# Kernel optimization log

Measured on AMD Instinct MI355X. Metric: run time of the kernel, lower is better.

The kernel has to match this reference:

```python
import jax, jax.numpy as jnp
import numpy as np
import math

B, S, D, H = 2, 2048, 1024, 16
DH = D // H

def setup_inputs() -> dict:
    key = jax.random.key(0)
    k = jax.random.split(key, 6)
    scale = 1.0 / math.sqrt(D)
    x = jax.random.normal(k[0], (B, S, D), jnp.float32)
    mask = jnp.ones((B, S), jnp.int32)
    # torch.nn.Linear weights: [out_features, in_features]
    W_q = jax.random.normal(k[1], (D, D), jnp.float32) * scale
    b_q = jnp.zeros((D,), jnp.float32)
    W_v = jax.random.normal(k[2], (D, D), jnp.float32) * scale
    W_out = jax.random.normal(k[3], (D, D), jnp.float32) * scale
    b_out = jnp.zeros((D,), jnp.float32)
    return {"x": x, "W_q": W_q, "b_q": b_q, "W_v": W_v, "W_out": W_out, "b_out": b_out, "mask": mask}

def reference(x, W_q, b_q, W_v, W_out, b_out, mask):
    inv_sqrt_dh = 1.0 / math.sqrt(DH)
    # q: [B, H, S, DH]
    q = (x @ W_q.T + b_q).reshape(B, S, H, DH).transpose(0, 2, 1, 3)
    # L2-distance attention logits: -(||q_s||^2 - 2 q_s.q_t + ||q_t||^2)/sqrt(dh)
    sq = jnp.sum(q * q, axis=-1)  # [B, H, S]
    qk = jnp.einsum('bhsd,bhtd->bhst', q, q)  # [B, H, S, S]
    logits = -(sq[..., :, None] - 2.0 * qk + sq[..., None, :]) * inv_sqrt_dh
    logits = jnp.where(mask[:, None, None, :] == 0, jnp.float32(-9e15), logits)
    w = jax.nn.softmax(logits, axis=-1)  # [B, H, S, S]
    # W_q_T[h, j, i] = W_q[i, h*DH + j] -> [H, DH, D]
    W_q_T = W_q.reshape(D, H, DH).transpose(1, 2, 0)
    # v[h, i, j] = W_v[i, h*DH + j] -> [H, D, DH]
    v = W_v.reshape(D, H, DH).transpose(1, 0, 2)
    attn = jnp.einsum('bhst,bhtd->bhsd', w, q)          # [B, H, S, DH]
    attn = jnp.einsum('bhsd,hde->bhse', attn, W_q_T)    # [B, H, S, D]
    attn = jnp.einsum('bhse,hef->bhsf', attn, v) * inv_sqrt_dh  # [B, H, S, DH]
    attn = attn.transpose(0, 2, 1, 3).reshape(B, S, D)
    return x + attn @ W_out.T + b_out
```

## Files before the change

### kernel.cpp

```cpp
#include <hip/hip_runtime.h>

#define S_LEN 2048
#define D_DIM 1024
#define NH    16
#define DHEAD 64

typedef float f32x4 __attribute__((ext_vector_type(4)));
typedef __bf16 bf16x8 __attribute__((ext_vector_type(8)));
typedef unsigned short u16;
typedef unsigned int u32;
typedef unsigned short u16x8 __attribute__((ext_vector_type(8)));
typedef unsigned short u16x4 __attribute__((ext_vector_type(4)));

__device__ __forceinline__ u16 f2bf(float f) {
    union { float f; unsigned u; } c; c.f = f;
    unsigned u = c.u + 0x7fffu + ((c.u >> 16) & 1u);
    return (u16)(u >> 16);
}

__device__ __forceinline__ u32 cvtpk(float lo, float hi) {
    u32 r;
    asm("v_cvt_pk_bf16_f32 %0, %1, %2" : "=v"(r) : "v"(lo), "v"(hi));
    return r;
}

__device__ __forceinline__ u32 pack_bf(float lo, float hi) {
    union { float f; u32 u; } a, b; a.f = lo; b.f = hi;
    return (b.u & 0xFFFF0000u) | (a.u >> 16);
}

#if __has_builtin(__builtin_amdgcn_exp2f)
#define EXP2(x) __builtin_amdgcn_exp2f(x)
#else
#define EXP2(x) exp2f(x)
#endif

#define C_QK  0.36067376022224085f
#define C_SQ  0.18033688011112043f

#define MFMA16(a, b, c) __builtin_amdgcn_mfma_f32_16x16x32_bf16((a), (b), (c), 0, 0, 0)

__global__ __launch_bounds__(256) void k_prep(
    const float* __restrict__ x, const float* __restrict__ Wq,
    u16* __restrict__ xbf, u16* __restrict__ Wqbf) {
    const size_t NX = (size_t)2 * S_LEN * D_DIM / 8;
    const size_t NW = (size_t)D_DIM * D_DIM / 8;
    for (size_t c = (size_t)blockIdx.x * 256 + threadIdx.x; c < NX + NW;
         c += (size_t)gridDim.x * 256) {
        const float* src; u16* dst; size_t off;
        if (c < NX) { src = x;  dst = xbf;  off = c * 8; }
        else        { src = Wq; dst = Wqbf; off = (c - NX) * 8; }
        f32x4 a = *(const f32x4*)(src + off);
        f32x4 b = *(const f32x4*)(src + off + 4);
        union { u32 w[4]; u16x8 v; } o;
        o.w[0] = cvtpk(a[0], a[1]); o.w[1] = cvtpk(a[2], a[3]);
        o.w[2] = cvtpk(b[0], b[1]); o.w[3] = cvtpk(b[2], b[3]);
        *(u16x8*)(dst + off) = o.v;
    }
}

__global__ __launch_bounds__(512, 4) void k_mega1(
    const u16* __restrict__ xbf, const u16* __restrict__ Wqbf,
    const float* __restrict__ Wq, const float* __restrict__ Wv,
    const float* __restrict__ bq, const int* __restrict__ mask,
    u16* __restrict__ Qbf, u16* __restrict__ QT,
    float* __restrict__ sq05, float* __restrict__ Mpart) {
    __shared__ __align__(16) char smem[38912];
    const int tid = threadIdx.x;

    if (blockIdx.x >= 256) {
        const int id = blockIdx.x - 256;
        const int z = id & 7, h = id >> 3;
        float* Qp = (float*)smem;
        float* Vp = (float*)(smem + 16384);
        const int r = tid >> 3, seg = tid & 7;
        const int j0 = (tid >> 4) * 2;
        const int f0 = (tid & 15) * 4;
        f32x4 acc0 = {0.f, 0.f, 0.f, 0.f}, acc1 = acc0;
        for (int c = 0; c < 2; ++c) {
            const int e0 = z * 128 + c * 64;
            __syncthreads();
            const float* q = Wq + (size_t)(e0 + r) * D_DIM + h * DHEAD + seg * 8;
            const float* v = Wv + (size_t)(e0 + r) * D_DIM + h * DHEAD + seg * 8;
            *(f32x4*)&Qp[r * 64 + seg * 8]     = *(const f32x4*)q;
            *(f32x4*)&Qp[r * 64 + seg * 8 + 4] = *(const f32x4*)(q + 4);
            *(f32x4*)&Vp[r * 64 + seg * 8]     = *(const f32x4*)v;
            *(f32x4*)&Vp[r * 64 + seg * 8 + 4] = *(const f32x4*)(v + 4);
            __syncthreads();
#pragma unroll 8
            for (int e = 0; e < 64; ++e) {
                float q0 = Qp[e * 64 + j0], q1 = Qp[e * 64 + j0 + 1];
                f32x4 vv = *(const f32x4*)&Vp[e * 64 + f0];
                acc0 += q0 * vv;
                acc1 += q1 * vv;
            }
        }
        float* dst = Mpart + (size_t)z * 65536 + ((size_t)(h * 64 + j0)) * 64 + f0;
        *(f32x4*)dst        = acc0 * 0.125f;
        *(f32x4*)(dst + 64) = acc1 * 0.125f;
        return;
    }

    u16* Al = (u16*)smem;
    u16* Bl = (u16*)(smem + 18432);
    float* sqp = (float*)(smem + 36864);

    const int lane = tid & 63, w = tid >> 6;
    const int wm = w & 1, wn = w >> 1;
    const int col16 = lane & 15, quad = lane >> 4;
    const int bm = blockIdx.x & 31, bn = blockIdx.x >> 5;

    f32x4 acc[4][2];
    const f32x4 z4 = {0.f, 0.f, 0.f, 0.f};
#pragma unroll
    for (int i = 0; i < 4; ++i)
#pragma unroll
        for (int j = 0; j < 2; ++j) acc[i][j] = z4;

    const int ar = tid >> 2, as = tid & 3;
    const u16* pa = xbf + (size_t)(bm * 128 + ar) * D_DIM + as * 16;
    const u16* pb = Wqbf + (size_t)(bn * 128 + ar) * D_DIM + as * 16;

    u16x8 ra[2], rb[2];
#pragma unroll
    for (int i = 0; i < 2; ++i) ra[i] = *(const u16x8*)(pa + i * 8);
#pragma unroll
    for (int i = 0; i < 2; ++i) rb[i] = *(const u16x8*)(pb + i * 8);

    for (int k0 = 0; k0 < D_DIM; k0 += 64) {
        __syncthreads();
#pragma unroll
        for (int i = 0; i < 2; ++i) *(u16x8*)&Al[ar * 72 + as * 16 + i * 8] = ra[i];
#pragma unroll
        for (int i = 0; i < 2; ++i) *(u16x8*)&Bl[ar * 72 + as * 16 + i * 8] = rb[i];
        __syncthreads();
        if (k0 + 64 < D_DIM) {
#pragma unroll
            for (int i = 0; i < 2; ++i) ra[i] = *(const u16x8*)(pa + k0 + 64 + i * 8);
#pragma unroll
            for (int i = 0; i < 2; ++i) rb[i] = *(const u16x8*)(pb + k0 + 64 + i * 8);
        }
#pragma unroll
        for (int kh = 0; kh < 2; ++kh) {
            bf16x8 af[4];
#pragma unroll
            for (int mt = 0; mt < 4; ++mt)
                af[mt] = *(const bf16x8*)&Al[(wm * 64 + mt * 16 + col16) * 72 + kh * 32 + quad * 8];
#pragma unroll
            for (int nt = 0; nt < 2; ++nt) {
                bf16x8 bfr = *(const bf16x8*)&Bl[(wn * 32 + nt * 16 + col16) * 72 + kh * 32 + quad * 8];
#pragma unroll
                for (int mt = 0; mt < 4; ++mt)
                    acc[mt][nt] = MFMA16(af[mt], bfr, acc[mt][nt]);
            }
        }
    }

    const int hh = wn >> 1;
    f32x4 ssum[4];
#pragma unroll
    for (int mt = 0; mt < 4; ++mt) ssum[mt] = z4;

    u16 qv16[2][4][4];
#pragma unroll
    for (int nt = 0; nt < 2; ++nt) {
        int col = bn * 128 + wn * 32 + nt * 16 + col16;
        float bqv = bq[col];
#pragma unroll
        for (int mt = 0; mt < 4; ++mt) {
            int row0 = bm * 128 + wm * 64 + mt * 16 + quad * 4;
#pragma unroll
            for (int rr = 0; rr < 4; ++rr) {
                float qv = acc[mt][nt][rr] + bqv;
                ssum[mt][rr] += qv * qv;
                u16 bv = f2bf(qv);
                qv16[nt][mt][rr] = bv;
                Qbf[(size_t)(row0 + rr) * D_DIM + col] = bv;
            }
        }
    }
    float vred[4][4];
#pragma unroll
    for (int mt = 0; mt < 4; ++mt)
#pragma unroll
        for (int rr = 0; rr < 4; ++rr) {
            float v = ssum[mt][rr];
            v += __shfl_xor(v, 1); v += __shfl_xor(v, 2);
            v += __shfl_xor(v, 4); v += __shfl_xor(v, 8);
            vred[mt][rr] = v;
        }
    if (col16 == 0) {
#pragma unroll
        for (int mt = 0; mt < 4; ++mt)
#pragma unroll
            for (int rr = 0; rr < 4; ++rr)
                sqp[wn * 128 + wm * 64 + mt * 16 + quad * 4 + rr] = vred[mt][rr];
    }
    __syncthreads();

    u16* Td = (u16*)smem;
#pragma unroll
    for (int nt = 0; nt < 2; ++nt) {
        int dloc = (wn & 1) * 32 + nt * 16 + col16;
#pragma unroll
        for (int mt = 0; mt < 4; ++mt) {
            int sl = wm * 64 + mt * 16 + quad * 4;
#pragma unroll
            for (int rr = 0; rr < 4; ++rr)
                Td[(hh * 64 + dloc) * 130 + sl + rr] = qv16[nt][mt][rr];
        }
    }
    __syncthreads();

    const int bb = (bm * 128) >> 11, s0 = (bm * 128) & 2047;
    if (tid < 256) {
        int r = tid & 127, hh2 = tid >> 7;
        float v = sqp[(2 * hh2) * 128 + r] + sqp[(2 * hh2 + 1) * 128 + r];
        int sidx = s0 + r;
        float o = mask[bb * S_LEN + sidx] ? v * C_SQ : 1e30f;
        sq05[((size_t)(bb * NH + bn * 2 + hh2)) * S_LEN + sidx] = o;
    }
    {
        int dr = tid >> 2, ch = tid & 3;
        int hh3 = dr >> 6, d = dr & 63;
        u16* dst = QT + ((size_t)(bb * NH + bn * 2 + hh3) * DHEAD + d) * S_LEN + s0 + ch * 32;
        const u16* src = Td + (hh3 * 64 + d) * 130 + ch * 32;
#pragma unroll
        for (int i = 0; i < 4; ++i)
            *(u16x8*)(dst + i * 8) = *(const u16x8*)(src + i * 8);
    }
}

__global__ __launch_bounds__(256, 2) void k_mega2(
    const u16* __restrict__ Qbf, const u16* __restrict__ QT,
    const float* __restrict__ sq05, u16* __restrict__ attnO,
    const float* __restrict__ Mpart, const float* __restrict__ Wout,
    u16* __restrict__ W2) {
    __shared__ __align__(16) char smem[34816];
    const int tid = threadIdx.x;

    if (blockIdx.x >= 512) {
        const int id = blockIdx.x - 512;
        const int ob = id & 15, h = id >> 4;
        float* Ms = (float*)smem;
        float* Ws = (float*)(smem + 16640);
        {
            int rr = tid >> 2, seg = tid & 3;
            const size_t mo = ((size_t)(h * 64 + rr)) * 64 + seg * 16;
            const float* ws = Wout + (size_t)(ob * 64 + rr) * D_DIM + h * DHEAD + seg * 16;
#pragma unroll
            for (int e = 0; e < 16; ++e) {
                float s = 0.f;
#pragma unroll
                for (int k = 0; k < 8; ++k) s += Mpart[mo + e + (size_t)k * 65536];
                Ms[rr * 65 + seg * 16 + e] = s;
                Ws[rr * 65 + seg * 16 + e] = ws[e];
            }
        }
        __syncthreads();
        int j = tid & 63, o0 = (tid >> 6) * 16;
        for (int oo = o0; oo < o0 + 16; ++oo) {
            float acc = 0.f;
#pragma unroll
            for (int f = 0; f < 64; ++f) acc += Ms[j * 65 + f] * Ws[oo * 65 + f];
            W2[(size_t)(ob * 64 + oo) * D_DIM + h * DHEAD + j] = f2bf(acc);
        }
        return;
    }

    u16* Kt  = (u16*)smem;
    u16* KtT = (u16*)(smem + 16384);
    float* sql = (float*)(smem + 32768);

    const int lane = tid & 63, w = tid >> 6;
    const int col16 = lane & 15, quad = lane >> 4;
    const int wq = w & 1, wk = w >> 1;
    const int bh = blockIdx.x & 31;
    const int qt = blockIdx.x >> 5;
    const int h = bh & 15;
    const int b = bh >> 4;
    const u16* qbase = Qbf + (size_t)b * S_LEN * D_DIM + h * DHEAD;
    const u16* qtbase = QT + ((size_t)(b * NH + h)) * DHEAD * S_LEN;
    const float* sqb = sq05 + ((size_t)(b * NH + h)) * S_LEN;

    bf16x8 qb[4][2];
#pragma unroll
    for (int nq = 0; nq < 4; ++nq)
#pragma unroll
        for (int k0 = 0; k0 < 2; ++k0)
            qb[nq][k0] = *(const bf16x8*)(qbase +
                (size_t)(qt * 128 + wq * 64 + nq * 16 + col16) * D_DIM + k0 * 32 + quad * 8);

    const int r00 = wk * 64 + (col16 >> 2) * 8 + (col16 & 3);
    const int swzA = (col16 & 3) | (((col16 >> 2) & 1) << 2);
    const int krow00 = r00 * 64 + (quad ^ swzA) * 8;
    const int sq00 = wk * 64 + quad * 8;
    int vrow[4];
#pragma unroll
    for (int dblk = 0; dblk < 4; ++dblk) {
        int rT = dblk * 16 + col16;
        vrow[dblk] = rT * 128 + ((wk * 8 + quad) ^ (rT & 7)) * 8;
    }

    const int kr = tid >> 1, ks = tid & 1;
    const int td = tid >> 2, ts = tid & 3;
    const int kswz = (kr & 3) | (((kr >> 3) & 1) << 2);
    const int tswz = td & 7;
    const u16* ksrc = qbase + (size_t)kr * D_DIM + ks * 32;
    const u16* tsrc = qtbase + (size_t)td * S_LEN + ts * 32;

    u16x8 pk[4], pt[4];
    float sv = 0.f;
#pragma unroll
    for (int i = 0; i < 4; ++i) pk[i] = *(const u16x8*)(ksrc + i * 8);
#pragma unroll
    for (int i = 0; i < 4; ++i) pt[i] = *(const u16x8*)(tsrc + i * 8);
    if (tid < 128) sv = sqb[tid];

    f32x4 Oacc[4][4], lacc[4];
    const f32x4 z4 = {0.f, 0.f, 0.f, 0.f};
#pragma unroll
    for (int n = 0; n < 4; ++n) {
        lacc[n] = z4;
#pragma unroll
        for (int d = 0; d < 4; ++d) Oacc[d][n] = z4;
    }
    bf16x8 ones;
    {
        union { u16x8 u; bf16x8 b; } cv;
#pragma unroll
        for (int e = 0; e < 8; ++e) cv.u[e] = 0x3F80;
        ones = cv.b;
    }

    for (int j = 0; j < S_LEN / 128; ++j) {
        __syncthreads();
#pragma unroll
        for (int i = 0; i < 4; ++i)
            *(u16x8*)(Kt + kr * 64 + ((ks * 4 + i) ^ kswz) * 8) = pk[i];
#pragma unroll
        for (int i = 0; i < 4; ++i)
            *(u16x8*)(KtT + td * 128 + ((ts * 4 + i) ^ tswz) * 8) = pt[i];
        if (tid < 128) sql[tid] = sv;
        __syncthreads();

        int jn = (j + 1) & 15;
        {
            const u16* kn = ksrc + (size_t)jn * 128 * D_DIM;
            const u16* tn = tsrc + (size_t)jn * 128;
#pragma unroll
            for (int i = 0; i < 4; ++i) pk[i] = *(const u16x8*)(kn + i * 8);
#pragma unroll
            for (int i = 0; i < 4; ++i) pt[i] = *(const u16x8*)(tn + i * 8);
            if (tid < 128) sv = sqb[jn * 128 + tid];
        }

        for (int kt = 0; kt < 2; ++kt) {
            f32x4 sacc[2][4];
#pragma unroll
            for (int kbh = 0; kbh < 2; ++kbh)
#pragma unroll
                for (int nq = 0; nq < 4; ++nq) sacc[kbh][nq] = z4;
#pragma unroll
            for (int kbh = 0; kbh < 2; ++kbh) {
                int kro = krow00 + kt * 2048 + kbh * 256;
                bf16x8 a0 = *(const bf16x8*)(Kt + kro);
                bf16x8 a1 = *(const bf16x8*)(Kt + (kro ^ 32));
#pragma unroll
                for (int nq = 0; nq < 4; ++nq) {
                    sacc[kbh][nq] = MFMA16(a0, qb[nq][0], sacc[kbh][nq]);
                    sacc[kbh][nq] = MFMA16(a1, qb[nq][1], sacc[kbh][nq]);
                }
            }

            bf16x8 va[4];
#pragma unroll
            for (int dblk = 0; dblk < 4; ++dblk)
                va[dblk] = *(const bf16x8*)(KtT + (vrow[dblk] ^ (kt * 32)));

            u32 pf[4][4];
#pragma unroll
            for (int kbh = 0; kbh < 2; ++kbh) {
                f32x4 sqv = *(const f32x4*)(sql + sq00 + kt * 32 + kbh * 4);
#pragma unroll
                for (int nq = 0; nq < 4; ++nq) {
                    float p0 = EXP2(fmaf(sacc[kbh][nq][0], C_QK, -sqv[0]));
                    float p1 = EXP2(fmaf(sacc[kbh][nq][1], C_QK, -sqv[1]));
                    float p2 = EXP2(fmaf(sacc[kbh][nq][2], C_QK, -sqv[2]));
                    float p3 = EXP2(fmaf(sacc[kbh][nq][3], C_QK, -sqv[3]));
                    pf[nq][kbh * 2]     = pack_bf(p0, p1);
                    pf[nq][kbh * 2 + 1] = pack_bf(p2, p3);
                }
            }

#pragma unroll
            for (int nq = 0; nq < 4; ++nq) {
                union { u32 u[4]; bf16x8 b; } pb;
#pragma unroll
                for (int i = 0; i < 4; ++i) pb.u[i] = pf[nq][i];
                lacc[nq] = MFMA16(ones, pb.b, lacc[nq]);
#pragma unroll
                for (int dblk = 0; dblk < 4; ++dblk)
                    Oacc[dblk][nq] = MFMA16(va[dblk], pb.b, Oacc[dblk][nq]);
            }
        }
    }

    __syncthreads();
    float* Obuf = (float*)smem;
    float* lred = (float*)(smem + 32768);
    if (wk == 1) {
#pragma unroll
        for (int dblk = 0; dblk < 4; ++dblk)
#pragma unroll
            for (int nq = 0; nq < 4; ++nq)
                *(f32x4*)(Obuf + ((wq * 16 + dblk * 4 + nq) * 64 + lane) * 4) = Oacc[dblk][nq];
#pragma unroll
        for (int nq = 0; nq < 4; ++nq)
            lred[(wq * 4 + nq) * 64 + lane] = lacc[nq][0];
    }
    __syncthreads();
    if (wk == 0) {
        float rinv[4];
#pragma unroll
        for (int nq = 0; nq < 4; ++nq)
            rinv[nq] = 1.f / (lacc[nq][0] + lred[(wq * 4 + nq) * 64 + lane]);
        u16* obase = attnO + (size_t)b * S_LEN * D_DIM + h * DHEAD;
#pragma unroll
        for (int dblk = 0; dblk < 4; ++dblk)
#pragma unroll
            for (int nq = 0; nq < 4; ++nq) {
                f32x4 o = Oacc[dblk][nq] + *(const f32x4*)(Obuf + ((wq * 16 + dblk * 4 + nq) * 64 + lane) * 4);
                int q = qt * 128 + wq * 64 + nq * 16 + col16;
                u16x4 pkk;
#pragma unroll
                for (int rr = 0; rr < 4; ++rr) pkk[rr] = f2bf(o[rr] * rinv[nq]);
                *(u16x4*)(obase + (size_t)q * D_DIM + dblk * 16 + quad * 4) = pkk;
            }
    }
}

__global__ __launch_bounds__(256, 4) void k_oproj(
    const u16* __restrict__ attnO, const u16* __restrict__ W2,
    const float* __restrict__ x, const float* __restrict__ bout, float* __restrict__ out) {
    __shared__ __align__(16) char smem[27648];
    u16* Al = (u16*)smem;
    u16* Bl = (u16*)(smem + 9216);
    const int tid = threadIdx.x, lane = tid & 63, wn = tid >> 6;
    const int col16 = lane & 15, quad = lane >> 4;
    const int bm = blockIdx.x, bn = blockIdx.y;

    f32x4 acc[4][2];
    const f32x4 z4 = {0.f, 0.f, 0.f, 0.f};
#pragma unroll
    for (int i = 0; i < 4; ++i)
#pragma unroll
        for (int j = 0; j < 2; ++j) acc[i][j] = z4;

    const int arA = tid >> 2, asA = tid & 3;
    const int brB = tid >> 1, bsB = tid & 1;
    const u16* pa = attnO + (size_t)(bm * 64 + arA) * D_DIM + asA * 16;
    const u16* pb = W2 + (size_t)(bn * 128 + brB) * D_DIM + bsB * 32;

    u16x8 ra[2], rb[4];
#pragma unroll
    for (int i = 0; i < 2; ++i) ra[i] = *(const u16x8*)(pa + i * 8);
#pragma unroll
    for (int i = 0; i < 4; ++i) rb[i] = *(const u16x8*)(pb + i * 8);

    for (int k0 = 0; k0 < D_DIM; k0 += 64) {
        __syncthreads();
#pragma unroll
        for (int i = 0; i < 2; ++i) *(u16x8*)&Al[arA * 72 + asA * 16 + i * 8] = ra[i];
#pragma unroll
        for (int i = 0; i < 4; ++i) *(u16x8*)&Bl[brB * 72 + bsB * 32 + i * 8] = rb[i];
        __syncthreads();
        if (k0 + 64 < D_DIM) {
#pragma unroll
            for (int i = 0; i < 2; ++i) ra[i] = *(const u16x8*)(pa + k0 + 64 + i * 8);
#pragma unroll
            for (int i = 0; i < 4; ++i) rb[i] = *(const u16x8*)(pb + k0 + 64 + i * 8);
        }
#pragma unroll
        for (int kh = 0; kh < 2; ++kh) {
            bf16x8 af[4];
#pragma unroll
            for (int mt = 0; mt < 4; ++mt)
                af[mt] = *(const bf16x8*)&Al[(mt * 16 + col16) * 72 + kh * 32 + quad * 8];
#pragma unroll
            for (int nt = 0; nt < 2; ++nt) {
                bf16x8 bfr = *(const bf16x8*)&Bl[(wn * 32 + nt * 16 + col16) * 72 + kh * 32 + quad * 8];
#pragma unroll
                for (int mt = 0; mt < 4; ++mt)
                    acc[mt][nt] = MFMA16(af[mt], bfr, acc[mt][nt]);
            }
        }
    }
#pragma unroll
    for (int nt = 0; nt < 2; ++nt) {
        int col = bn * 128 + wn * 32 + nt * 16 + col16;
        float bv = bout[col];
#pragma unroll
        for (int mt = 0; mt < 4; ++mt) {
            int row0 = bm * 64 + mt * 16 + quad * 4;
#pragma unroll
            for (int rr = 0; rr < 4; ++rr) {
                size_t idx = (size_t)(row0 + rr) * D_DIM + col;
                out[idx] = acc[mt][nt][rr] + x[idx] + bv;
            }
        }
    }
}

extern "C" void kernel_launch(void* const* d_in, const int* in_sizes, int n_in,
                              void* d_out, int out_size, void* d_ws, size_t ws_size,
                              hipStream_t stream) {
    const float* x    = (const float*)d_in[0];
    const float* Wq   = (const float*)d_in[1];
    const float* bq   = (const float*)d_in[2];
    const float* Wv   = (const float*)d_in[3];
    const float* Wout = (const float*)d_in[4];
    const float* bout = (const float*)d_in[5];
    const int*   mask = (const int*)d_in[6];
    float* out = (float*)d_out;

    char* ws = (char*)d_ws;
    u16*   Qbf   = (u16*)(ws);
    u16*   QT    = (u16*)(ws + (8u << 20));
    u16*   attnO = (u16*)(ws + (16u << 20));
    u16*   W2    = (u16*)(ws + (24u << 20));
    float* Mpart = (float*)(ws + (26u << 20));
    float* sq05  = (float*)(ws + (28u << 20));
    u16*   xbf   = attnO;
    u16*   Wqbf  = W2;

    k_prep<<<dim3(2048), dim3(256), 0, stream>>>(x, Wq, xbf, Wqbf);
    k_mega1<<<dim3(384), dim3(512), 0, stream>>>(xbf, Wqbf, Wq, Wv, bq, mask, Qbf, QT, sq05, Mpart);
    k_mega2<<<dim3(768), dim3(256), 0, stream>>>(Qbf, QT, sq05, attnO, Mpart, Wout, W2);
    k_oproj<<<dim3(64, 8), dim3(256), 0, stream>>>(attnO, W2, x, bout, out);
}
```

Before: 178.4 us.

## Split attention key tiles across four wave groups with 512-thread blocks

The attention kernel now runs 8 waves per block instead of 4. Each key-wave group handles one 32-key slice of every 128-key tile, rather than two 64-key halves processed in a kt loop. The partial O and l accumulators from three wave groups are reduced through shared memory one dblk at a time, which adds extra barriers. The goal is more waves in flight and a shorter serial inner loop per wave, to better hide latency. The cost is more reduction traffic and synchronisation in the epilogue, plus tighter register pressure under launch bounds of (512, 4).

```diff
diff --git a/kernel.cpp b/kernel.cpp
--- a/kernel.cpp
+++ b/kernel.cpp
@@ -231,7 +231,7 @@
     }
 }
 
-__global__ __launch_bounds__(256, 2) void k_mega2(
+__global__ __launch_bounds__(512, 4) void k_mega2(
     const u16* __restrict__ Qbf, const u16* __restrict__ QT,
     const float* __restrict__ sq05, u16* __restrict__ attnO,
     const float* __restrict__ Mpart, const float* __restrict__ Wout,
@@ -245,21 +245,21 @@
         float* Ms = (float*)smem;
         float* Ws = (float*)(smem + 16640);
         {
-            int rr = tid >> 2, seg = tid & 3;
-            const size_t mo = ((size_t)(h * 64 + rr)) * 64 + seg * 16;
-            const float* ws = Wout + (size_t)(ob * 64 + rr) * D_DIM + h * DHEAD + seg * 16;
-#pragma unroll
-            for (int e = 0; e < 16; ++e) {
+            int rr = tid >> 3, seg = tid & 7;
+            const size_t mo = ((size_t)(h * 64 + rr)) * 64 + seg * 8;
+            const float* ws = Wout + (size_t)(ob * 64 + rr) * D_DIM + h * DHEAD + seg * 8;
+#pragma unroll
+            for (int e = 0; e < 8; ++e) {
                 float s = 0.f;
 #pragma unroll
                 for (int k = 0; k < 8; ++k) s += Mpart[mo + e + (size_t)k * 65536];
-                Ms[rr * 65 + seg * 16 + e] = s;
-                Ws[rr * 65 + seg * 16 + e] = ws[e];
-            }
-        }
-        __syncthreads();
-        int j = tid & 63, o0 = (tid >> 6) * 16;
-        for (int oo = o0; oo < o0 + 16; ++oo) {
+                Ms[rr * 65 + seg * 8 + e] = s;
+                Ws[rr * 65 + seg * 8 + e] = ws[e];
+            }
+        }
+        __syncthreads();
+        int j = tid & 63, o0 = (tid >> 6) * 8;
+        for (int oo = o0; oo < o0 + 8; ++oo) {
             float acc = 0.f;
 #pragma unroll
             for (int f = 0; f < 64; ++f) acc += Ms[j * 65 + f] * Ws[oo * 65 + f];
@@ -291,30 +291,30 @@
             qb[nq][k0] = *(const bf16x8*)(qbase +
                 (size_t)(qt * 128 + wq * 64 + nq * 16 + col16) * D_DIM + k0 * 32 + quad * 8);
 
-    const int r00 = wk * 64 + (col16 >> 2) * 8 + (col16 & 3);
+    const int r00 = wk * 32 + (col16 >> 2) * 8 + (col16 & 3);
     const int swzA = (col16 & 3) | (((col16 >> 2) & 1) << 2);
     const int krow00 = r00 * 64 + (quad ^ swzA) * 8;
-    const int sq00 = wk * 64 + quad * 8;
+    const int sq00 = wk * 32 + quad * 8;
     int vrow[4];
 #pragma unroll
     for (int dblk = 0; dblk < 4; ++dblk) {
         int rT = dblk * 16 + col16;
-        vrow[dblk] = rT * 128 + ((wk * 8 + quad) ^ (rT & 7)) * 8;
-    }
-
-    const int kr = tid >> 1, ks = tid & 1;
-    const int td = tid >> 2, ts = tid & 3;
+        vrow[dblk] = rT * 128 + ((wk * 4 + quad) ^ (rT & 7)) * 8;
+    }
+
+    const int kr = tid >> 2, ks = tid & 3;
+    const int td = tid >> 3, ts = tid & 7;
     const int kswz = (kr & 3) | (((kr >> 3) & 1) << 2);
     const int tswz = td & 7;
-    const u16* ksrc = qbase + (size_t)kr * D_DIM + ks * 32;
-    const u16* tsrc = qtbase + (size_t)td * S_LEN + ts * 32;
-
-    u16x8 pk[4], pt[4];
+    const u16* ksrc = qbase + (size_t)kr * D_DIM + ks * 16;
+    const u16* tsrc = qtbase + (size_t)td * S_LEN + ts * 16;
+
+    u16x8 pk[2], pt[2];
     float sv = 0.f;
 #pragma unroll
-    for (int i = 0; i < 4; ++i) pk[i] = *(const u16x8*)(ksrc + i * 8);
-#pragma unroll
-    for (int i = 0; i < 4; ++i) pt[i] = *(const u16x8*)(tsrc + i * 8);
+    for (int i = 0; i < 2; ++i) pk[i] = *(const u16x8*)(ksrc + i * 8);
+#pragma unroll
+    for (int i = 0; i < 2; ++i) pt[i] = *(const u16x8*)(tsrc + i * 8);
     if (tid < 128) sv = sqb[tid];
 
     f32x4 Oacc[4][4], lacc[4];
@@ -336,11 +336,11 @@
     for (int j = 0; j < S_LEN / 128; ++j) {
         __syncthreads();
 #pragma unroll
-        for (int i = 0; i < 4; ++i)
-            *(u16x8*)(Kt + kr * 64 + ((ks * 4 + i) ^ kswz) * 8) = pk[i];
-#pragma unroll
-        for (int i = 0; i < 4; ++i)
-            *(u16x8*)(KtT + td * 128 + ((ts * 4 + i) ^ tswz) * 8) = pt[i];
+        for (int i = 0; i < 2; ++i)
+            *(u16x8*)(Kt + kr * 64 + ((ks * 2 + i) ^ kswz) * 8) = pk[i];
+#pragma unroll
+        for (int i = 0; i < 2; ++i)
+            *(u16x8*)(KtT + td * 128 + ((ts * 2 + i) ^ tswz) * 8) = pt[i];
         if (tid < 128) sql[tid] = sv;
         __syncthreads();
 
@@ -349,94 +349,101 @@
             const u16* kn = ksrc + (size_t)jn * 128 * D_DIM;
             const u16* tn = tsrc + (size_t)jn * 128;
 #pragma unroll
-            for (int i = 0; i < 4; ++i) pk[i] = *(const u16x8*)(kn + i * 8);
-#pragma unroll
-            for (int i = 0; i < 4; ++i) pt[i] = *(const u16x8*)(tn + i * 8);
+            for (int i = 0; i < 2; ++i) pk[i] = *(const u16x8*)(kn + i * 8);
+#pragma unroll
+            for (int i = 0; i < 2; ++i) pt[i] = *(const u16x8*)(tn + i * 8);
             if (tid < 128) sv = sqb[jn * 128 + tid];
         }
 
-        for (int kt = 0; kt < 2; ++kt) {
-            f32x4 sacc[2][4];
-#pragma unroll
-            for (int kbh = 0; kbh < 2; ++kbh)
-#pragma unroll
-                for (int nq = 0; nq < 4; ++nq) sacc[kbh][nq] = z4;
-#pragma unroll
-            for (int kbh = 0; kbh < 2; ++kbh) {
-                int kro = krow00 + kt * 2048 + kbh * 256;
-                bf16x8 a0 = *(const bf16x8*)(Kt + kro);
-                bf16x8 a1 = *(const bf16x8*)(Kt + (kro ^ 32));
-#pragma unroll
-                for (int nq = 0; nq < 4; ++nq) {
-                    sacc[kbh][nq] = MFMA16(a0, qb[nq][0], sacc[kbh][nq]);
-                    sacc[kbh][nq] = MFMA16(a1, qb[nq][1], sacc[kbh][nq]);
-                }
-            }
-
-            bf16x8 va[4];
+        f32x4 sacc[2][4];
+#pragma unroll
+        for (int kbh = 0; kbh < 2; ++kbh)
+#pragma unroll
+            for (int nq = 0; nq < 4; ++nq) sacc[kbh][nq] = z4;
+#pragma unroll
+        for (int kbh = 0; kbh < 2; ++kbh) {
+            int kro = krow00 + kbh * 256;
+            bf16x8 a0 = *(const bf16x8*)(Kt + kro);
+            bf16x8 a1 = *(const bf16x8*)(Kt + (kro ^ 32));
+#pragma unroll
+            for (int nq = 0; nq < 4; ++nq) {
+                sacc[kbh][nq] = MFMA16(a0, qb[nq][0], sacc[kbh][nq]);
+                sacc[kbh][nq] = MFMA16(a1, qb[nq][1], sacc[kbh][nq]);
+            }
+        }
+
+        bf16x8 va[4];
+#pragma unroll
+        for (int dblk = 0; dblk < 4; ++dblk)
+            va[dblk] = *(const bf16x8*)(KtT + vrow[dblk]);
+
+        u32 pf[4][4];
+#pragma unroll
+        for (int kbh = 0; kbh < 2; ++kbh) {
+            f32x4 sqv = *(const f32x4*)(sql + sq00 + kbh * 4);
+#pragma unroll
+            for (int nq = 0; nq < 4; ++nq) {
+                float p0 = EXP2(fmaf(sacc[kbh][nq][0], C_QK, -sqv[0]));
+                float p1 = EXP2(fmaf(sacc[kbh][nq][1], C_QK, -sqv[1]));
+                float p2 = EXP2(fmaf(sacc[kbh][nq][2], C_QK, -sqv[2]));
+                float p3 = EXP2(fmaf(sacc[kbh][nq][3], C_QK, -sqv[3]));
+                pf[nq][kbh * 2]     = pack_bf(p0, p1);
+                pf[nq][kbh * 2 + 1] = pack_bf(p2, p3);
+            }
+        }
+
+#pragma unroll
+        for (int nq = 0; nq < 4; ++nq) {
+            union { u32 u[4]; bf16x8 b; } pb;
+#pragma unroll
+            for (int i = 0; i < 4; ++i) pb.u[i] = pf[nq][i];
+            lacc[nq] = MFMA16(ones, pb.b, lacc[nq]);
 #pragma unroll
             for (int dblk = 0; dblk < 4; ++dblk)
-                va[dblk] = *(const bf16x8*)(KtT + (vrow[dblk] ^ (kt * 32)));
-
-            u32 pf[4][4];
-#pragma unroll
-            for (int kbh = 0; kbh < 2; ++kbh) {
-                f32x4 sqv = *(const f32x4*)(sql + sq00 + kt * 32 + kbh * 4);
-#pragma unroll
-                for (int nq = 0; nq < 4; ++nq) {
-                    float p0 = EXP2(fmaf(sacc[kbh][nq][0], C_QK, -sqv[0]));
-                    float p1 = EXP2(fmaf(sacc[kbh][nq][1], C_QK, -sqv[1]));
-                    float p2 = EXP2(fmaf(sacc[kbh][nq][2], C_QK, -sqv[2]));
-                    float p3 = EXP2(fmaf(sacc[kbh][nq][3], C_QK, -sqv[3]));
-                    pf[nq][kbh * 2]     = pack_bf(p0, p1);
-                    pf[nq][kbh * 2 + 1] = pack_bf(p2, p3);
-                }
-            }
-
-#pragma unroll
-            for (int nq = 0; nq < 4; ++nq) {
-                union { u32 u[4]; bf16x8 b; } pb;
-#pragma unroll
-                for (int i = 0; i < 4; ++i) pb.u[i] = pf[nq][i];
-                lacc[nq] = MFMA16(ones, pb.b, lacc[nq]);
-#pragma unroll
-                for (int dblk = 0; dblk < 4; ++dblk)
-                    Oacc[dblk][nq] = MFMA16(va[dblk], pb.b, Oacc[dblk][nq]);
-            }
+                Oacc[dblk][nq] = MFMA16(va[dblk], pb.b, Oacc[dblk][nq]);
         }
     }
 
     __syncthreads();
     float* Obuf = (float*)smem;
-    float* lred = (float*)(smem + 32768);
-    if (wk == 1) {
-#pragma unroll
-        for (int dblk = 0; dblk < 4; ++dblk)
+    float* lred = (float*)(smem + 24576);
+    if (wk) {
+#pragma unroll
+        for (int nq = 0; nq < 4; ++nq)
+            lred[(((wk - 1) * 2 + wq) * 4 + nq) * 64 + lane] = lacc[nq][0];
+    }
+    float rinv[4];
+    u16* obase = attnO + (size_t)b * S_LEN * D_DIM + h * DHEAD;
+    for (int dblk = 0; dblk < 4; ++dblk) {
+        if (wk) {
 #pragma unroll
             for (int nq = 0; nq < 4; ++nq)
-                *(f32x4*)(Obuf + ((wq * 16 + dblk * 4 + nq) * 64 + lane) * 4) = Oacc[dblk][nq];
-#pragma unroll
-        for (int nq = 0; nq < 4; ++nq)
-            lred[(wq * 4 + nq) * 64 + lane] = lacc[nq][0];
-    }
-    __syncthreads();
-    if (wk == 0) {
-        float rinv[4];
-#pragma unroll
-        for (int nq = 0; nq < 4; ++nq)
-            rinv[nq] = 1.f / (lacc[nq][0] + lred[(wq * 4 + nq) * 64 + lane]);
-        u16* obase = attnO + (size_t)b * S_LEN * D_DIM + h * DHEAD;
-#pragma unroll
-        for (int dblk = 0; dblk < 4; ++dblk)
+                *(f32x4*)(Obuf + ((((wk - 1) * 2 + wq) * 4 + nq) * 64 + lane) * 4) = Oacc[dblk][nq];
+        }
+        __syncthreads();
+        if (!wk) {
+            if (dblk == 0) {
+#pragma unroll
+                for (int nq = 0; nq < 4; ++nq)
+                    rinv[nq] = 1.f / (lacc[nq][0]
+                        + lred[((0 * 2 + wq) * 4 + nq) * 64 + lane]
+                        + lred[((1 * 2 + wq) * 4 + nq) * 64 + lane]
+                        + lred[((2 * 2 + wq) * 4 + nq) * 64 + lane]);
+            }
 #pragma unroll
             for (int nq = 0; nq < 4; ++nq) {
-                f32x4 o = Oacc[dblk][nq] + *(const f32x4*)(Obuf + ((wq * 16 + dblk * 4 + nq) * 64 + lane) * 4);
+                f32x4 o = Oacc[dblk][nq];
+#pragma unroll
+                for (int m = 0; m < 3; ++m)
+                    o += *(const f32x4*)(Obuf + (((m * 2 + wq) * 4 + nq) * 64 + lane) * 4);
                 int q = qt * 128 + wq * 64 + nq * 16 + col16;
                 u16x4 pkk;
 #pragma unroll
                 for (int rr = 0; rr < 4; ++rr) pkk[rr] = f2bf(o[rr] * rinv[nq]);
                 *(u16x4*)(obase + (size_t)q * D_DIM + dblk * 16 + quad * 4) = pkk;
             }
+        }
+        __syncthreads();
     }
 }
 
@@ -536,6 +543,6 @@
 
     k_prep<<<dim3(2048), dim3(256), 0, stream>>>(x, Wq, xbf, Wqbf);
     k_mega1<<<dim3(384), dim3(512), 0, stream>>>(xbf, Wqbf, Wq, Wv, bq, mask, Qbf, QT, sq05, Mpart);
-    k_mega2<<<dim3(768), dim3(256), 0, stream>>>(Qbf, QT, sq05, attnO, Mpart, Wout, W2);
+    k_mega2<<<dim3(768), dim3(512), 0, stream>>>(Qbf, QT, sq05, attnO, Mpart, Wout, W2);
     k_oproj<<<dim3(64, 8), dim3(256), 0, stream>>>(attnO, W2, x, bout, out);
 }
```

Result: slower. 451.6 us (+153.1%).

## Halve k_mega1 block size and use 64-row GEMM tiles for more blocks

Applied to the files above, without the earlier changes.

k_mega1 now runs with 256-thread blocks. The Q-projection GEMM tile shrinks from 128x128 to 64x128, so the grid grows from 256 to 512 GEMM blocks. The Wq*Wv side blocks now compute 4 output rows per thread instead of 2, so 256 threads cover the same 64x64 product. The goal is more blocks and better occupancy and wave balance across the CUs. In exchange, each A/B tile is reused less and the global loads of the Wq tile are duplicated across twice as many M-blocks.

```diff
diff --git a/kernel.cpp b/kernel.cpp
--- a/kernel.cpp
+++ b/kernel.cpp
@@ -59,56 +59,59 @@
     }
 }
 
-__global__ __launch_bounds__(512, 4) void k_mega1(
+__global__ __launch_bounds__(256, 4) void k_mega1(
     const u16* __restrict__ xbf, const u16* __restrict__ Wqbf,
     const float* __restrict__ Wq, const float* __restrict__ Wv,
     const float* __restrict__ bq, const int* __restrict__ mask,
     u16* __restrict__ Qbf, u16* __restrict__ QT,
     float* __restrict__ sq05, float* __restrict__ Mpart) {
-    __shared__ __align__(16) char smem[38912];
+    __shared__ __align__(16) char smem[33792];
     const int tid = threadIdx.x;
 
-    if (blockIdx.x >= 256) {
-        const int id = blockIdx.x - 256;
+    if (blockIdx.x >= 512) {
+        const int id = blockIdx.x - 512;
         const int z = id & 7, h = id >> 3;
         float* Qp = (float*)smem;
         float* Vp = (float*)(smem + 16384);
-        const int r = tid >> 3, seg = tid & 7;
-        const int j0 = (tid >> 4) * 2;
+        const int r = tid >> 2, seg = tid & 3;
+        const int j0 = (tid >> 4) * 4;
         const int f0 = (tid & 15) * 4;
-        f32x4 acc0 = {0.f, 0.f, 0.f, 0.f}, acc1 = acc0;
+        f32x4 acc[4];
+#pragma unroll
+        for (int jj = 0; jj < 4; ++jj) acc[jj] = (f32x4){0.f, 0.f, 0.f, 0.f};
         for (int c = 0; c < 2; ++c) {
             const int e0 = z * 128 + c * 64;
             __syncthreads();
-            const float* q = Wq + (size_t)(e0 + r) * D_DIM + h * DHEAD + seg * 8;
-            const float* v = Wv + (size_t)(e0 + r) * D_DIM + h * DHEAD + seg * 8;
-            *(f32x4*)&Qp[r * 64 + seg * 8]     = *(const f32x4*)q;
-            *(f32x4*)&Qp[r * 64 + seg * 8 + 4] = *(const f32x4*)(q + 4);
-            *(f32x4*)&Vp[r * 64 + seg * 8]     = *(const f32x4*)v;
-            *(f32x4*)&Vp[r * 64 + seg * 8 + 4] = *(const f32x4*)(v + 4);
+            const float* q = Wq + (size_t)(e0 + r) * D_DIM + h * DHEAD + seg * 16;
+            const float* v = Wv + (size_t)(e0 + r) * D_DIM + h * DHEAD + seg * 16;
+#pragma unroll
+            for (int i = 0; i < 4; ++i) {
+                *(f32x4*)&Qp[r * 64 + seg * 16 + i * 4] = *(const f32x4*)(q + i * 4);
+                *(f32x4*)&Vp[r * 64 + seg * 16 + i * 4] = *(const f32x4*)(v + i * 4);
+            }
             __syncthreads();
-#pragma unroll 8
+#pragma unroll 4
             for (int e = 0; e < 64; ++e) {
-                float q0 = Qp[e * 64 + j0], q1 = Qp[e * 64 + j0 + 1];
                 f32x4 vv = *(const f32x4*)&Vp[e * 64 + f0];
-                acc0 += q0 * vv;
-                acc1 += q1 * vv;
+#pragma unroll
+                for (int jj = 0; jj < 4; ++jj)
+                    acc[jj] += Qp[e * 64 + j0 + jj] * vv;
             }
         }
         float* dst = Mpart + (size_t)z * 65536 + ((size_t)(h * 64 + j0)) * 64 + f0;
-        *(f32x4*)dst        = acc0 * 0.125f;
-        *(f32x4*)(dst + 64) = acc1 * 0.125f;
+#pragma unroll
+        for (int jj = 0; jj < 4; ++jj)
+            *(f32x4*)(dst + (size_t)jj * 64) = acc[jj] * 0.125f;
         return;
     }
 
     u16* Al = (u16*)smem;
-    u16* Bl = (u16*)(smem + 18432);
-    float* sqp = (float*)(smem + 36864);
-
-    const int lane = tid & 63, w = tid >> 6;
-    const int wm = w & 1, wn = w >> 1;
+    u16* Bl = (u16*)(smem + 9216);
+    float* sqp = (float*)(smem + 27648);
+
+    const int lane = tid & 63, wn = tid >> 6;
     const int col16 = lane & 15, quad = lane >> 4;
-    const int bm = blockIdx.x & 31, bn = blockIdx.x >> 5;
+    const int bm = blockIdx.x & 63, bn = blockIdx.x >> 6;
 
     f32x4 acc[4][2];
     const f32x4 z4 = {0.f, 0.f, 0.f, 0.f};
@@ -117,35 +120,36 @@
 #pragma unroll
         for (int j = 0; j < 2; ++j) acc[i][j] = z4;
 
-    const int ar = tid >> 2, as = tid & 3;
-    const u16* pa = xbf + (size_t)(bm * 128 + ar) * D_DIM + as * 16;
-    const u16* pb = Wqbf + (size_t)(bn * 128 + ar) * D_DIM + as * 16;
-
-    u16x8 ra[2], rb[2];
+    const int arA = tid >> 2, asA = tid & 3;
+    const int brB = tid >> 1, bsB = tid & 1;
+    const u16* pa = xbf + (size_t)(bm * 64 + arA) * D_DIM + asA * 16;
+    const u16* pb = Wqbf + (size_t)(bn * 128 + brB) * D_DIM + bsB * 32;
+
+    u16x8 ra[2], rb[4];
 #pragma unroll
     for (int i = 0; i < 2; ++i) ra[i] = *(const u16x8*)(pa + i * 8);
 #pragma unroll
-    for (int i = 0; i < 2; ++i) rb[i] = *(const u16x8*)(pb + i * 8);
+    for (int i = 0; i < 4; ++i) rb[i] = *(const u16x8*)(pb + i * 8);
 
     for (int k0 = 0; k0 < D_DIM; k0 += 64) {
         __syncthreads();
 #pragma unroll
-        for (int i = 0; i < 2; ++i) *(u16x8*)&Al[ar * 72 + as * 16 + i * 8] = ra[i];
-#pragma unroll
-        for (int i = 0; i < 2; ++i) *(u16x8*)&Bl[ar * 72 + as * 16 + i * 8] = rb[i];
+        for (int i = 0; i < 2; ++i) *(u16x8*)&Al[arA * 72 + asA * 16 + i * 8] = ra[i];
+#pragma unroll
+        for (int i = 0; i < 4; ++i) *(u16x8*)&Bl[brB * 72 + bsB * 32 + i * 8] = rb[i];
         __syncthreads();
         if (k0 + 64 < D_DIM) {
 #pragma unroll
             for (int i = 0; i < 2; ++i) ra[i] = *(const u16x8*)(pa + k0 + 64 + i * 8);
 #pragma unroll
-            for (int i = 0; i < 2; ++i) rb[i] = *(const u16x8*)(pb + k0 + 64 + i * 8);
+            for (int i = 0; i < 4; ++i) rb[i] = *(const u16x8*)(pb + k0 + 64 + i * 8);
         }
 #pragma unroll
         for (int kh = 0; kh < 2; ++kh) {
             bf16x8 af[4];
 #pragma unroll
             for (int mt = 0; mt < 4; ++mt)
-                af[mt] = *(const bf16x8*)&Al[(wm * 64 + mt * 16 + col16) * 72 + kh * 32 + quad * 8];
+                af[mt] = *(const bf16x8*)&Al[(mt * 16 + col16) * 72 + kh * 32 + quad * 8];
 #pragma unroll
             for (int nt = 0; nt < 2; ++nt) {
                 bf16x8 bfr = *(const bf16x8*)&Bl[(wn * 32 + nt * 16 + col16) * 72 + kh * 32 + quad * 8];
@@ -168,7 +172,7 @@
         float bqv = bq[col];
 #pragma unroll
         for (int mt = 0; mt < 4; ++mt) {
-            int row0 = bm * 128 + wm * 64 + mt * 16 + quad * 4;
+            int row0 = bm * 64 + mt * 16 + quad * 4;
 #pragma unroll
             for (int rr = 0; rr < 4; ++rr) {
                 float qv = acc[mt][nt][rr] + bqv;
@@ -194,7 +198,7 @@
         for (int mt = 0; mt < 4; ++mt)
 #pragma unroll
             for (int rr = 0; rr < 4; ++rr)
-                sqp[wn * 128 + wm * 64 + mt * 16 + quad * 4 + rr] = vred[mt][rr];
+                sqp[wn * 64 + mt * 16 + quad * 4 + rr] = vred[mt][rr];
     }
     __syncthreads();
 
@@ -204,27 +208,27 @@
         int dloc = (wn & 1) * 32 + nt * 16 + col16;
 #pragma unroll
         for (int mt = 0; mt < 4; ++mt) {
-            int sl = wm * 64 + mt * 16 + quad * 4;
+            int sl = mt * 16 + quad * 4;
 #pragma unroll
             for (int rr = 0; rr < 4; ++rr)
-                Td[(hh * 64 + dloc) * 130 + sl + rr] = qv16[nt][mt][rr];
+                Td[(hh * 64 + dloc) * 66 + sl + rr] = qv16[nt][mt][rr];
         }
     }
     __syncthreads();
 
-    const int bb = (bm * 128) >> 11, s0 = (bm * 128) & 2047;
-    if (tid < 256) {
-        int r = tid & 127, hh2 = tid >> 7;
-        float v = sqp[(2 * hh2) * 128 + r] + sqp[(2 * hh2 + 1) * 128 + r];
+    const int bb = bm >> 5, s0 = (bm * 64) & 2047;
+    if (tid < 128) {
+        int r = tid & 63, hh2 = tid >> 6;
+        float v = sqp[(2 * hh2) * 64 + r] + sqp[(2 * hh2 + 1) * 64 + r];
         int sidx = s0 + r;
         float o = mask[bb * S_LEN + sidx] ? v * C_SQ : 1e30f;
         sq05[((size_t)(bb * NH + bn * 2 + hh2)) * S_LEN + sidx] = o;
     }
     {
-        int dr = tid >> 2, ch = tid & 3;
+        int dr = tid >> 1, ch = tid & 1;
         int hh3 = dr >> 6, d = dr & 63;
         u16* dst = QT + ((size_t)(bb * NH + bn * 2 + hh3) * DHEAD + d) * S_LEN + s0 + ch * 32;
-        const u16* src = Td + (hh3 * 64 + d) * 130 + ch * 32;
+        const u16* src = Td + (hh3 * 64 + d) * 66 + ch * 32;
 #pragma unroll
         for (int i = 0; i < 4; ++i)
             *(u16x8*)(dst + i * 8) = *(const u16x8*)(src + i * 8);
@@ -535,7 +539,7 @@
     u16*   Wqbf  = W2;
 
     k_prep<<<dim3(2048), dim3(256), 0, stream>>>(x, Wq, xbf, Wqbf);
-    k_mega1<<<dim3(384), dim3(512), 0, stream>>>(xbf, Wqbf, Wq, Wv, bq, mask, Qbf, QT, sq05, Mpart);
+    k_mega1<<<dim3(640), dim3(256), 0, stream>>>(xbf, Wqbf, Wq, Wv, bq, mask, Qbf, QT, sq05, Mpart);
     k_mega2<<<dim3(768), dim3(256), 0, stream>>>(Qbf, QT, sq05, attnO, Mpart, Wout, W2);
     k_oproj<<<dim3(64, 8), dim3(256), 0, stream>>>(attnO, W2, x, bout, out);
 }
```

Measured after the change: 179.0 us. About the same (+0.3%).
